# Optimization experiments

Hardware: AMD Instinct MI355X
Metric: run time of the kernel (lower is better)

Reference implementation:

```python
import jax, jax.numpy as jnp
import numpy as np

TEMPERATURE = 0.02


def setup_inputs() -> dict:
    key = jax.random.key(0)
    k1, k2 = jax.random.split(key)
    B, D_PER, DIM = 4096, 2, 1024
    # scale embeddings so sim/temperature stays in a sane range (like normalized embeddings)
    scale = 1.0 / np.sqrt(DIM)
    query_embeds = jax.random.normal(k1, (B, DIM), dtype=jnp.float32) * scale
    doc_embeds = jax.random.normal(k2, (B * D_PER, DIM), dtype=jnp.float32) * scale
    return {
        "query_embeds": query_embeds,
        "doc_embeds": doc_embeds,
        "num_docs_per_sample": D_PER,
    }


def reference(query_embeds, doc_embeds, num_docs_per_sample):
    # Single-device path of the original: all_doc_embeds == doc_embeds,
    # local_rank == 0, pos_global_idx = i * num_docs_per_sample.
    B = query_embeds.shape[0]
    # [B, total_docs] similarity matrix (one batched GEMM instead of per-sample loop)
    logits = (query_embeds @ doc_embeds.T) / TEMPERATURE
    pos_idx = jnp.arange(B) * num_docs_per_sample  # constant docs-per-sample offsets
    pos_logit = jnp.take_along_axis(logits, pos_idx[:, None], axis=1)[:, 0]
    lse = jax.nn.logsumexp(logits, axis=1)
    loss = jnp.sum(lse - pos_logit) / B
    return loss
```

## Files before the change

### kernel.cpp

```cpp
#include <hip/hip_runtime.h>


#define TEMP_INV 50.0f
#define PRESCALE 16.0f
#define SCALE_BYTE 123

typedef int   i32x4 __attribute__((ext_vector_type(4)));
typedef int   i32x8 __attribute__((ext_vector_type(8)));
typedef float f32x4 __attribute__((ext_vector_type(4)));

__global__ void cvt_kernel(const float* __restrict__ Q, const float* __restrict__ Dm,
                           unsigned int* __restrict__ Q8, unsigned int* __restrict__ D8,
                           float* __restrict__ rowsum, int qSlots, int B, int K) {
    const int gid = blockIdx.x * blockDim.x + threadIdx.x;
    if (gid < B) rowsum[gid] = 0.0f;
    const float* src;
    unsigned int* dst;
    int s;
    if (gid < qSlots) { src = Q;  dst = Q8; s = gid; }
    else              { src = Dm; dst = D8; s = gid - qSlots; }
    const int l   = s & 63;
    const int c   = (s >> 6) & 15;
    const int k0b = (s >> 10) & 7;
    const int R   = s >> 13;
    const int row = R * 128 + (c >> 1) * 16 + (l & 15);
    const int k   = k0b * 128 + (c & 1) * 64 + (l >> 4) * 16;
    const float* p = src + (size_t)row * K + k;
    unsigned int w[4];
#pragma unroll
    for (int d = 0; d < 4; ++d) {
        float4 v = *(const float4*)(p + d * 4);
        int t = __builtin_amdgcn_cvt_pk_fp8_f32(v.x * PRESCALE, v.y * PRESCALE, 0, false);
        t = __builtin_amdgcn_cvt_pk_fp8_f32(v.z * PRESCALE, v.w * PRESCALE, t, true);
        w[d] = (unsigned int)t;
    }
    *(uint4*)(dst + (size_t)s * 4) = make_uint4(w[0], w[1], w[2], w[3]);
}

__global__ __launch_bounds__(256, 2) void gemm_expsum_kernel(
        const unsigned int* __restrict__ Q8, const unsigned int* __restrict__ D8,
        const int* __restrict__ dper,
        float* __restrict__ rowsum, float* __restrict__ pos, int K) {
    __shared__ unsigned int Qs[4096];
    __shared__ unsigned int Ds[4096];

    const int tid   = threadIdx.x;
    const int wave  = tid >> 6;
    const int lane  = tid & 63;
    const int lquad = lane >> 4;
    const int lm    = lane & 15;
    const int qbase = blockIdx.x * 128;
    const int dbase = blockIdx.y * 128;
    const int KB    = K >> 7;

    const int slotofs = ((lquad & 1) * 32 + lm) * 4;
    const int aofs = ((wave >> 1) * 8 + (lquad >> 1)) * 256 + slotofs;
    const int bofs = ((wave & 1) * 8 + (lquad >> 1)) * 256 + slotofs;

    const unsigned int* Qg = Q8 + (size_t)blockIdx.x * KB * 4096;
    const unsigned int* Dg = D8 + (size_t)blockIdx.y * KB * 4096;

    f32x4 acc[16];
#pragma unroll
    for (int t = 0; t < 16; ++t) acc[t] = (f32x4){0.f, 0.f, 0.f, 0.f};

    for (int kb = 0; kb < KB; ++kb) {
#pragma unroll
        for (int q = 0; q < 4; ++q) {
            const int c = wave * 4 + q;
            const unsigned int* g1 = Qg + kb * 4096 + c * 256 + lane * 4;
            __builtin_amdgcn_global_load_lds(
                (const __attribute__((address_space(1))) void*)g1,
                (__attribute__((address_space(3))) void*)(Qs + c * 256 + lane * 4),
                16, 0, 0);
            const unsigned int* g2 = Dg + kb * 4096 + c * 256 + lane * 4;
            __builtin_amdgcn_global_load_lds(
                (const __attribute__((address_space(1))) void*)g2,
                (__attribute__((address_space(3))) void*)(Ds + c * 256 + lane * 4),
                16, 0, 0);
        }
        __syncthreads();

        i32x8 a8[4], b8[4];
#pragma unroll
        for (int i = 0; i < 4; ++i) {
            i32x4 lo = *(const i32x4*)(Qs + aofs + i * 512);
            i32x4 hi = *(const i32x4*)(Qs + aofs + i * 512 + 64);
            a8[i] = __builtin_shufflevector(lo, hi, 0, 1, 2, 3, 4, 5, 6, 7);
        }
#pragma unroll
        for (int j = 0; j < 4; ++j) {
            i32x4 lo = *(const i32x4*)(Ds + bofs + j * 512);
            i32x4 hi = *(const i32x4*)(Ds + bofs + j * 512 + 64);
            b8[j] = __builtin_shufflevector(lo, hi, 0, 1, 2, 3, 4, 5, 6, 7);
        }
#pragma unroll
        for (int i = 0; i < 4; ++i)
#pragma unroll
            for (int j = 0; j < 4; ++j)
                acc[i * 4 + j] = __builtin_amdgcn_mfma_scale_f32_16x16x128_f8f6f4(
                    a8[i], b8[j], acc[i * 4 + j], 0, 0, 0, SCALE_BYTE, 0, SCALE_BYTE);
        __syncthreads();
    }

    const int dp = dper[0];
#pragma unroll
    for (int i = 0; i < 4; ++i)
#pragma unroll
        for (int r = 0; r < 4; ++r) {
            const int gr   = qbase + (wave >> 1) * 64 + 16 * i + 4 * lquad + r;
            const int pcol = gr * dp - dbase;
            float e = 0.0f;
#pragma unroll
            for (int j = 0; j < 4; ++j) {
                float v = acc[i * 4 + j][r];
                if ((wave & 1) * 64 + 16 * j + lm == pcol) pos[gr] = v * TEMP_INV;
                e += __expf(v * TEMP_INV);
            }
            e += __shfl_xor(e, 1);
            e += __shfl_xor(e, 2);
            e += __shfl_xor(e, 4);
            e += __shfl_xor(e, 8);
            if (lm == 0) atomicAdd(&rowsum[gr], e);
        }
}

__global__ void final_kernel(const float* __restrict__ rowsum,
                             const float* __restrict__ pos,
                             float* __restrict__ out, int B) {
    __shared__ float red[16];
    int tid = threadIdx.x;
    float s = 0.0f;
    for (int i = tid; i < B; i += blockDim.x)
        s += __logf(rowsum[i]) - pos[i];
    s += __shfl_xor(s, 32);
    s += __shfl_xor(s, 16);
    s += __shfl_xor(s, 8);
    s += __shfl_xor(s, 4);
    s += __shfl_xor(s, 2);
    s += __shfl_xor(s, 1);
    int w = tid >> 6, l = tid & 63;
    if (l == 0) red[w] = s;
    __syncthreads();
    if (tid == 0) {
        float t = 0.0f;
        int nw = blockDim.x >> 6;
        for (int i = 0; i < nw; ++i) t += red[i];
        out[0] = t / (float)B;
    }
}

extern "C" void kernel_launch(void* const* d_in, const int* in_sizes, int n_in,
                              void* d_out, int out_size, void* d_ws, size_t ws_size,
                              hipStream_t stream) {
    const float* Q   = (const float*)d_in[0];
    const float* Dm  = (const float*)d_in[1];
    const int* dper  = (const int*)d_in[2];
    float* out = (float*)d_out;

    const int DIM  = 1024;
    const int B    = in_sizes[0] / DIM;
    const int Ntot = in_sizes[1] / DIM;

    unsigned int* Q8 = (unsigned int*)d_ws;
    unsigned int* D8 = Q8 + (size_t)B * DIM / 4;
    float* rowsum = (float*)(D8 + (size_t)Ntot * DIM / 4);
    float* pos = rowsum + B;

    const int qSlots = B * DIM / 16;
    const int dSlots = Ntot * DIM / 16;
    cvt_kernel<<<(qSlots + dSlots) / 256, 256, 0, stream>>>(
        Q, Dm, Q8, D8, rowsum, qSlots, B, DIM);

    dim3 grid(B / 128, Ntot / 128);
    gemm_expsum_kernel<<<grid, 256, 0, stream>>>(Q8, D8, dper, rowsum, pos, DIM);

    final_kernel<<<1, 1024, 0, stream>>>(rowsum, pos, out, B);
}
```

Baseline: 127.7 us.

## Fuse final reduction into GEMM via last-block counter and XCD-aware tile mapping

Removes the separate final_kernel launch by adding one extra block to the GEMM grid. That block spins on a global completion counter and then performs the log-sum and mean reduction. It also remaps the 1D block index so that blocks landing on the same XCD share Q and D tiles, aiming for better L2 reuse. The cost is a spin-waiting block that occupies a CU slot. The design also relies on relaxed atomics for visibility, and the block index remap hardcodes a 32x64 grid shape.

```diff
diff --git a/kernel.cpp b/kernel.cpp
--- a/kernel.cpp
+++ b/kernel.cpp
@@ -4,6 +4,7 @@
 #define TEMP_INV 50.0f
 #define PRESCALE 16.0f
 #define SCALE_BYTE 123
+#define KD 1024
 
 typedef int   i32x4 __attribute__((ext_vector_type(4)));
 typedef int   i32x8 __attribute__((ext_vector_type(8)));
@@ -11,9 +12,11 @@
 
 __global__ void cvt_kernel(const float* __restrict__ Q, const float* __restrict__ Dm,
                            unsigned int* __restrict__ Q8, unsigned int* __restrict__ D8,
-                           float* __restrict__ rowsum, int qSlots, int B, int K) {
+                           float* __restrict__ rowsum, unsigned int* __restrict__ cnt,
+                           int qSlots, int B, int K) {
     const int gid = blockIdx.x * blockDim.x + threadIdx.x;
     if (gid < B) rowsum[gid] = 0.0f;
+    if (gid == 0) cnt[0] = 0u;
     const float* src;
     unsigned int* dst;
     int s;
@@ -40,25 +43,63 @@
 __global__ __launch_bounds__(256, 2) void gemm_expsum_kernel(
         const unsigned int* __restrict__ Q8, const unsigned int* __restrict__ D8,
         const int* __restrict__ dper,
-        float* __restrict__ rowsum, float* __restrict__ pos, int K) {
+        float* __restrict__ rowsum, float* __restrict__ pos,
+        unsigned int* __restrict__ cnt, float* __restrict__ out,
+        int B, int K, int W) {
     __shared__ unsigned int Qs[4096];
     __shared__ unsigned int Ds[4096];
+    __shared__ float redf[4];
 
     const int tid   = threadIdx.x;
     const int wave  = tid >> 6;
     const int lane  = tid & 63;
+
+    if ((int)blockIdx.x == W) {
+        if (tid == 0) {
+            while (__hip_atomic_load(cnt, __ATOMIC_RELAXED,
+                                     __HIP_MEMORY_SCOPE_AGENT) < (unsigned)W)
+                __builtin_amdgcn_s_sleep(2);
+        }
+        __syncthreads();
+        float s = 0.0f;
+        for (int i = tid; i < B; i += 256) {
+            float rs = __hip_atomic_load(&rowsum[i], __ATOMIC_RELAXED,
+                                         __HIP_MEMORY_SCOPE_AGENT);
+            float ps = __hip_atomic_load(&pos[i], __ATOMIC_RELAXED,
+                                         __HIP_MEMORY_SCOPE_AGENT);
+            s += __logf(rs) - ps;
+        }
+        s += __shfl_xor(s, 32);
+        s += __shfl_xor(s, 16);
+        s += __shfl_xor(s, 8);
+        s += __shfl_xor(s, 4);
+        s += __shfl_xor(s, 2);
+        s += __shfl_xor(s, 1);
+        if (lane == 0) redf[wave] = s;
+        __syncthreads();
+        if (tid == 0)
+            out[0] = (redf[0] + redf[1] + redf[2] + redf[3]) / (float)B;
+        return;
+    }
+
+    const int id  = blockIdx.x;
+    const int xcd = id & 7;
+    const int sl  = id >> 3;
+    const int bx  = (xcd & 3) * 8 + (sl & 7);
+    const int by  = (xcd >> 2) * 32 + (sl >> 3);
+
     const int lquad = lane >> 4;
     const int lm    = lane & 15;
-    const int qbase = blockIdx.x * 128;
-    const int dbase = blockIdx.y * 128;
+    const int qbase = bx * 128;
+    const int dbase = by * 128;
     const int KB    = K >> 7;
 
     const int slotofs = ((lquad & 1) * 32 + lm) * 4;
     const int aofs = ((wave >> 1) * 8 + (lquad >> 1)) * 256 + slotofs;
     const int bofs = ((wave & 1) * 8 + (lquad >> 1)) * 256 + slotofs;
 
-    const unsigned int* Qg = Q8 + (size_t)blockIdx.x * KB * 4096;
-    const unsigned int* Dg = D8 + (size_t)blockIdx.y * KB * 4096;
+    const unsigned int* Qg = Q8 + (size_t)bx * KB * 4096;
+    const unsigned int* Dg = D8 + (size_t)by * KB * 4096;
 
     f32x4 acc[16];
 #pragma unroll
@@ -114,7 +155,9 @@
 #pragma unroll
             for (int j = 0; j < 4; ++j) {
                 float v = acc[i * 4 + j][r];
-                if ((wave & 1) * 64 + 16 * j + lm == pcol) pos[gr] = v * TEMP_INV;
+                if ((wave & 1) * 64 + 16 * j + lm == pcol)
+                    __hip_atomic_store(&pos[gr], v * TEMP_INV, __ATOMIC_RELAXED,
+                                       __HIP_MEMORY_SCOPE_AGENT);
                 e += __expf(v * TEMP_INV);
             }
             e += __shfl_xor(e, 1);
@@ -123,31 +166,11 @@
             e += __shfl_xor(e, 8);
             if (lm == 0) atomicAdd(&rowsum[gr], e);
         }
-}
-
-__global__ void final_kernel(const float* __restrict__ rowsum,
-                             const float* __restrict__ pos,
-                             float* __restrict__ out, int B) {
-    __shared__ float red[16];
-    int tid = threadIdx.x;
-    float s = 0.0f;
-    for (int i = tid; i < B; i += blockDim.x)
-        s += __logf(rowsum[i]) - pos[i];
-    s += __shfl_xor(s, 32);
-    s += __shfl_xor(s, 16);
-    s += __shfl_xor(s, 8);
-    s += __shfl_xor(s, 4);
-    s += __shfl_xor(s, 2);
-    s += __shfl_xor(s, 1);
-    int w = tid >> 6, l = tid & 63;
-    if (l == 0) red[w] = s;
+
     __syncthreads();
-    if (tid == 0) {
-        float t = 0.0f;
-        int nw = blockDim.x >> 6;
-        for (int i = 0; i < nw; ++i) t += red[i];
-        out[0] = t / (float)B;
-    }
+    if (tid == 0)
+        __hip_atomic_fetch_add(cnt, 1u, __ATOMIC_RELAXED,
+                               __HIP_MEMORY_SCOPE_AGENT);
 }
 
 extern "C" void kernel_launch(void* const* d_in, const int* in_sizes, int n_in,
@@ -158,7 +181,7 @@
     const int* dper  = (const int*)d_in[2];
     float* out = (float*)d_out;
 
-    const int DIM  = 1024;
+    const int DIM  = KD;
     const int B    = in_sizes[0] / DIM;
     const int Ntot = in_sizes[1] / DIM;
 
@@ -166,14 +189,14 @@
     unsigned int* D8 = Q8 + (size_t)B * DIM / 4;
     float* rowsum = (float*)(D8 + (size_t)Ntot * DIM / 4);
     float* pos = rowsum + B;
+    unsigned int* cnt = (unsigned int*)(pos + B);
 
     const int qSlots = B * DIM / 16;
     const int dSlots = Ntot * DIM / 16;
     cvt_kernel<<<(qSlots + dSlots) / 256, 256, 0, stream>>>(
-        Q, Dm, Q8, D8, rowsum, qSlots, B, DIM);
-
-    dim3 grid(B / 128, Ntot / 128);
-    gemm_expsum_kernel<<<grid, 256, 0, stream>>>(Q8, D8, dper, rowsum, pos, DIM);
-
-    final_kernel<<<1, 1024, 0, stream>>>(rowsum, pos, out, B);
+        Q, Dm, Q8, D8, rowsum, cnt, qSlots, B, DIM);
+
+    const int W = (B / 128) * (Ntot / 128);
+    gemm_expsum_kernel<<<W + 1, 256, 0, stream>>>(Q8, D8, dper, rowsum, pos,
+                                                  cnt, out, B, DIM, W);
 }
```

New measurement: 145.8 us. 14.2% more time.
